# Kernel tuning notes

Hardware: AMD Instinct MI355X
Metric: run time of the kernel (lower is better)

## Reference

```python
import jax, jax.numpy as jnp
import numpy as np

DIM = 1024
HEADS = 16
MLP = 4096
EPS = 1e-5

def _layer_norm(x, g, b):
    mu = jnp.mean(x, axis=-1, keepdims=True)
    var = jnp.mean(jnp.square(x - mu), axis=-1, keepdims=True)
    return (x - mu) * jax.lax.rsqrt(var + EPS) * g + b

def setup_inputs() -> dict:
    key = jax.random.key(0)
    ks = jax.random.split(key, 8)
    s = 0.02
    return {
        "x": jax.random.normal(ks[0], (2, 2048, DIM), dtype=jnp.float32),
        "ln1_g": jnp.ones((DIM,), jnp.float32),
        "ln1_b": jnp.zeros((DIM,), jnp.float32),
        "qkv_w": jax.random.normal(ks[1], (DIM, 3 * DIM), jnp.float32) * s,
        "qkv_b": jnp.zeros((3 * DIM,), jnp.float32),
        "proj_w": jax.random.normal(ks[2], (DIM, DIM), jnp.float32) * s,
        "proj_b": jnp.zeros((DIM,), jnp.float32),
        "ln2_g": jnp.ones((DIM,), jnp.float32),
        "ln2_b": jnp.zeros((DIM,), jnp.float32),
        "fc1_w": jax.random.normal(ks[3], (DIM, MLP), jnp.float32) * s,
        "fc1_b": jnp.zeros((MLP,), jnp.float32),
        "fc2_w": jax.random.normal(ks[4], (MLP, DIM), jnp.float32) * s,
        "fc2_b": jnp.zeros((DIM,), jnp.float32),
    }

def reference(x, ln1_g, ln1_b, qkv_w, qkv_b, proj_w, proj_b,
              ln2_g, ln2_b, fc1_w, fc1_b, fc2_w, fc2_b):
    B, N, C = x.shape
    H = HEADS
    D = C // H
    # --- attention (pre-norm); NOTE: source applies no 1/sqrt(D) scaling ---
    h = _layer_norm(x, ln1_g, ln1_b)
    qkv = (h @ qkv_w + qkv_b).reshape(B, N, 3, H, D)
    q, k, v = (qkv[:, :, 0], qkv[:, :, 1], qkv[:, :, 2])  # [B,N,H,D]
    qk = jnp.einsum('bnhd,bmhd->bhnm', q, k)
    attn = jax.nn.softmax(qk, axis=-1)
    y = jnp.einsum('bhnm,bmhd->bnhd', attn, v).reshape(B, N, C)
    y = y @ proj_w + proj_b
    x = x + y
    # --- MLP (pre-norm), exact GELU like torch nn.GELU ---
    h2 = _layer_norm(x, ln2_g, ln2_b)
    h2 = jax.nn.gelu(h2 @ fc1_w + fc1_b, approximate=False)
    x = x + (h2 @ fc2_w + fc2_b)
    return x
```

## Files before the change

kernel.cpp:

```cpp
#include <hip/hip_runtime.h>
#include <hip/hip_bf16.h>

#define CDIM   1024
#define NSEQ   2048
#define NHEAD  16
#define HDIM   64
#define MLPDIM 4096
#define TROWS  4096

typedef __attribute__((ext_vector_type(8)))  __bf16 bf16x8;
typedef __attribute__((ext_vector_type(4)))  float  f32x4;
typedef __attribute__((ext_vector_type(16))) float  f32x16;
typedef __attribute__((ext_vector_type(4)))  unsigned short us4;

static __device__ __forceinline__ unsigned short f2bf(float f) {
  unsigned int u = __float_as_uint(f);
  u += 0x7fffu + ((u >> 16) & 1u);
  return (unsigned short)(u >> 16);
}

#define MFMA16(a, b, c) __builtin_amdgcn_mfma_f32_16x16x32_bf16(a, b, c, 0, 0, 0)
#define MFMA32(a, b, c) __builtin_amdgcn_mfma_f32_32x32x16_bf16(a, b, c, 0, 0, 0)

static __device__ __forceinline__ void gll16(const unsigned short* g, unsigned short* l) {
  __builtin_amdgcn_global_load_lds(
      (const __attribute__((address_space(1))) unsigned int*)g,
      (__attribute__((address_space(3))) unsigned int*)l, 16, 0, 0);
}

__global__ __launch_bounds__(256)
void ln_bf16_kernel(const float* __restrict__ x,
                    const float* __restrict__ gam,
                    const float* __restrict__ bet,
                    unsigned short* __restrict__ out)
{
  int row = blockIdx.x;
  int t = threadIdx.x;
  const float4* xr = (const float4*)(x + (size_t)row * CDIM);
  float4 v = xr[t];
  float s  = v.x + v.y + v.z + v.w;
  float s2 = v.x*v.x + v.y*v.y + v.z*v.z + v.w*v.w;
  #pragma unroll
  for (int off = 32; off > 0; off >>= 1) {
    s  += __shfl_down(s, off);
    s2 += __shfl_down(s2, off);
  }
  __shared__ float rs[4], rs2[4];
  int wave = t >> 6, lane = t & 63;
  if (lane == 0) { rs[wave] = s; rs2[wave] = s2; }
  __syncthreads();
  float fs  = rs[0] + rs[1] + rs[2] + rs[3];
  float fs2 = rs2[0] + rs2[1] + rs2[2] + rs2[3];
  float mu   = fs * (1.0f / CDIM);
  float var  = fs2 * (1.0f / CDIM) - mu * mu;
  float rstd = rsqrtf(var + 1e-5f);
  float4 gg = ((const float4*)gam)[t];
  float4 bb = ((const float4*)bet)[t];
  us4 o;
  o.x = f2bf((v.x - mu) * rstd * gg.x + bb.x);
  o.y = f2bf((v.y - mu) * rstd * gg.y + bb.y);
  o.z = f2bf((v.z - mu) * rstd * gg.z + bb.z);
  o.w = f2bf((v.w - mu) * rstd * gg.w + bb.w);
  ((us4*)(out + (size_t)row * CDIM))[t] = o;
}

__global__ __launch_bounds__(256)
void wt_bf16_kernel(const float* __restrict__ W, unsigned short* __restrict__ Wt,
                    int K, int N)
{
  __shared__ float tile[32][33];
  int n0 = blockIdx.x * 32, k0 = blockIdx.y * 32;
  int t = threadIdx.x;
  int r = t >> 3, c4 = (t & 7) << 2;
  float4 v = *(const float4*)(W + (size_t)(k0 + r) * N + n0 + c4);
  tile[r][c4 + 0] = v.x; tile[r][c4 + 1] = v.y;
  tile[r][c4 + 2] = v.z; tile[r][c4 + 3] = v.w;
  __syncthreads();
  us4 o;
  o.x = f2bf(tile[c4 + 0][r]);
  o.y = f2bf(tile[c4 + 1][r]);
  o.z = f2bf(tile[c4 + 2][r]);
  o.w = f2bf(tile[c4 + 3][r]);
  *(us4*)(Wt + (size_t)(n0 + r) * K + k0 + c4) = o;
}

template<int EPI>
__global__ __launch_bounds__(256, 2)
void gemm_bt(const unsigned short* __restrict__ A, const unsigned short* __restrict__ Bt,
             const float* __restrict__ bias, int M, int N, int K,
             float* __restrict__ outf, unsigned short* __restrict__ outb,
             const float* __restrict__ resid,
             unsigned short* __restrict__ qo, unsigned short* __restrict__ ko,
             unsigned short* __restrict__ vo)
{
  __shared__ unsigned short As[128 * 32];
  __shared__ unsigned short Bs[128 * 32];
  const int tid  = threadIdx.x;
  const int lane = tid & 63;
  const int wave = tid >> 6;
  const int wr = wave >> 1, wc = wave & 1;
  const int g = lane >> 4, r16 = lane & 15;
  const int bm = blockIdx.y * 128, bn = blockIdx.x * 128;

  f32x4 acc[4][4];
  #pragma unroll
  for (int i = 0; i < 4; i++)
    #pragma unroll
    for (int j = 0; j < 4; j++) acc[i][j] = (f32x4){0.f, 0.f, 0.f, 0.f};

  for (int k0 = 0; k0 < K; k0 += 32) {
    #pragma unroll
    for (int c = 0; c < 2; c++) {
      int o   = (c * 256 + tid) << 3;
      int row = o >> 5;
      int col = o & 31;
      int ub  = (c * 256 + (tid & ~63)) << 3;
      gll16(A  + (size_t)(bm + row) * K + k0 + col, &As[ub]);
      gll16(Bt + (size_t)(bn + row) * K + k0 + col, &Bs[ub]);
    }
    __syncthreads();
    bf16x8 af[4], bfr[4];
    #pragma unroll
    for (int i = 0; i < 4; i++) {
      int row = wr * 64 + i * 16 + r16;
      af[i] = *(const bf16x8*)(&As[row * 32 + 8 * g]);
    }
    #pragma unroll
    for (int j = 0; j < 4; j++) {
      int row = wc * 64 + j * 16 + r16;
      bfr[j] = *(const bf16x8*)(&Bs[row * 32 + 8 * g]);
    }
    #pragma unroll
    for (int i = 0; i < 4; i++)
      #pragma unroll
      for (int j = 0; j < 4; j++)
        acc[i][j] = MFMA16(af[i], bfr[j], acc[i][j]);
    __syncthreads();
  }

  #pragma unroll
  for (int i = 0; i < 4; i++) {
    #pragma unroll
    for (int j = 0; j < 4; j++) {
      int col = bn + wc * 64 + j * 16 + r16;
      float bv = bias[col];
      #pragma unroll
      for (int jj = 0; jj < 4; jj++) {
        int row = bm + wr * 64 + i * 16 + 4 * g + jj;
        float val = acc[i][j][jj] + bv;
        if (EPI == 1) {
          int sel = col >> 10, cc = col & 1023;
          int hh = cc >> 6, d = cc & 63;
          int b = row >> 11, tk = row & 2047;
          size_t hb = (size_t)(b * NHEAD + hh);
          if (sel == 0)      qo[(hb * NSEQ + tk) * HDIM + d] = f2bf(val * 1.4426950408889634f);
          else if (sel == 1) ko[(hb * NSEQ + tk) * HDIM + d] = f2bf(val);
          else               vo[(hb * HDIM + d) * NSEQ + tk] = f2bf(val);
        } else if (EPI == 2) {
          size_t idx = (size_t)row * N + col;
          outf[idx] = val + resid[idx];
        } else {
          float ge = 0.5f * val * (1.0f + erff(val * 0.70710678118654752f));
          outb[(size_t)row * N + col] = f2bf(ge);
        }
      }
    }
  }
}

__global__ __launch_bounds__(256, 2)
void attn_kernel(const unsigned short* __restrict__ q, const unsigned short* __restrict__ k,
                 const unsigned short* __restrict__ vt, unsigned short* __restrict__ y)
{
  int bid = blockIdx.x;
  int xcd = bid & 7, loc = bid >> 3;
  int bh  = xcd * 4 + (loc >> 4);
  int qblk = loc & 15;
  int b = bh >> 4, h = bh & 15;
  int wave = threadIdx.x >> 6, lane = threadIdx.x & 63;
  int ql = lane & 31;
  int hi = lane >> 5;
  int q0 = qblk * 128 + wave * 32;
  const unsigned short* qb = q  + (size_t)bh * NSEQ * HDIM;
  const unsigned short* kb = k  + (size_t)bh * NSEQ * HDIM;
  const unsigned short* vb = vt + (size_t)bh * HDIM * NSEQ;

  bf16x8 aq[4];
  #pragma unroll
  for (int s = 0; s < 4; s++)
    aq[s] = *(const bf16x8*)(qb + (size_t)(q0 + ql) * HDIM + s * 16 + hi * 8);

  float m = -1e30f, ssum = 0.f;
  f32x16 o0, o1;
  #pragma unroll
  for (int r = 0; r < 16; r++) { o0[r] = 0.f; o1[r] = 0.f; }

  bf16x8 kf[2][4];
  #pragma unroll
  for (int s = 0; s < 4; s++)
    kf[0][s] = *(const bf16x8*)(kb + (size_t)ql * HDIM + s * 16 + hi * 8);

  #pragma unroll 2
  for (int it = 0; it < NSEQ / 32; it++) {
    const int kv0 = it * 32;
    const int cur = it & 1, nxt = cur ^ 1;
    bf16x8 vf[2][2];
    #pragma unroll
    for (int t = 0; t < 2; t++)
      #pragma unroll
      for (int db = 0; db < 2; db++)
        vf[t][db] = *(const bf16x8*)(vb + (size_t)(db * 32 + ql) * NSEQ + kv0 + t * 16 + hi * 8);
    f32x16 sacc;
    #pragma unroll
    for (int r = 0; r < 16; r++) sacc[r] = 0.f;
    __builtin_amdgcn_s_setprio(1);
    #pragma unroll
    for (int s = 0; s < 4; s++)
      sacc = MFMA32(kf[cur][s], aq[s], sacc);
    __builtin_amdgcn_s_setprio(0);
    {
      int kvn = (kv0 + 32) & (NSEQ - 1);
      #pragma unroll
      for (int s = 0; s < 4; s++)
        kf[nxt][s] = *(const bf16x8*)(kb + (size_t)(kvn + ql) * HDIM + s * 16 + hi * 8);
    }
    float tmax = sacc[0];
    #pragma unroll
    for (int r = 1; r < 16; r++) tmax = fmaxf(tmax, sacc[r]);
    tmax = fmaxf(tmax, __shfl_xor(tmax, 32));
    float mn = fmaxf(m, tmax);
    float scale = exp2f(m - mn);
    m = mn;
    float ps = 0.f;
    #pragma unroll
    for (int r = 0; r < 16; r++) {
      sacc[r] = exp2f(sacc[r] - mn);
      ps += sacc[r];
    }
    ssum = ssum * scale + ps;
    #pragma unroll
    for (int r = 0; r < 16; r++) { o0[r] *= scale; o1[r] *= scale; }
    __builtin_amdgcn_s_setprio(1);
    #pragma unroll
    for (int t = 0; t < 2; t++) {
      unsigned pk01, pk23, pk45, pk67;
      asm("v_cvt_pk_bf16_f32 %0, %1, %2" : "=v"(pk01) : "v"(sacc[8*t+0]), "v"(sacc[8*t+1]));
      asm("v_cvt_pk_bf16_f32 %0, %1, %2" : "=v"(pk23) : "v"(sacc[8*t+2]), "v"(sacc[8*t+3]));
      asm("v_cvt_pk_bf16_f32 %0, %1, %2" : "=v"(pk45) : "v"(sacc[8*t+4]), "v"(sacc[8*t+5]));
      asm("v_cvt_pk_bf16_f32 %0, %1, %2" : "=v"(pk67) : "v"(sacc[8*t+6]), "v"(sacc[8*t+7]));
      asm("v_permlane32_swap_b32 %0, %1" : "+v"(pk01), "+v"(pk45));
      asm("v_permlane32_swap_b32 %0, %1" : "+v"(pk23), "+v"(pk67));
      union { unsigned u[4]; bf16x8 v; } pf;
      pf.u[0] = pk01; pf.u[1] = pk23; pf.u[2] = pk45; pf.u[3] = pk67;
      o0 = MFMA32(vf[t][0], pf.v, o0);
      o1 = MFMA32(vf[t][1], pf.v, o1);
    }
    __builtin_amdgcn_s_setprio(0);
  }
  float stot = ssum + __shfl_xor(ssum, 32);
  float inv = 1.0f / stot;
  unsigned short* yr = y + ((size_t)(b * NSEQ + q0 + ql)) * CDIM + h * HDIM;
  #pragma unroll
  for (int db = 0; db < 2; db++) {
    const f32x16& oo = db ? o1 : o0;
    #pragma unroll
    for (int rq = 0; rq < 4; rq++) {
      us4 w;
      w.x = f2bf(oo[4*rq+0] * inv);
      w.y = f2bf(oo[4*rq+1] * inv);
      w.z = f2bf(oo[4*rq+2] * inv);
      w.w = f2bf(oo[4*rq+3] * inv);
      *(us4*)(yr + db * 32 + rq * 8 + hi * 4) = w;
    }
  }
}

extern "C" void kernel_launch(void* const* d_in, const int* in_sizes, int n_in,
                              void* d_out, int out_size, void* d_ws, size_t ws_size,
                              hipStream_t stream)
{
  const float* x      = (const float*)d_in[0];
  const float* ln1_g  = (const float*)d_in[1];
  const float* ln1_b  = (const float*)d_in[2];
  const float* qkv_w  = (const float*)d_in[3];
  const float* qkv_b  = (const float*)d_in[4];
  const float* proj_w = (const float*)d_in[5];
  const float* proj_b = (const float*)d_in[6];
  const float* ln2_g  = (const float*)d_in[7];
  const float* ln2_b  = (const float*)d_in[8];
  const float* fc1_w  = (const float*)d_in[9];
  const float* fc1_b  = (const float*)d_in[10];
  const float* fc2_w  = (const float*)d_in[11];
  const float* fc2_b  = (const float*)d_in[12];
  float* out = (float*)d_out;

  char* p = (char*)d_ws;
  size_t off = 0;
  auto alloc = [&](size_t bytes) -> void* {
    void* r = p + off; off += (bytes + 255) & ~(size_t)255; return r;
  };
  unsigned short* wt_qkv  = (unsigned short*)alloc((size_t)3072 * 1024 * 2);
  unsigned short* wt_proj = (unsigned short*)alloc((size_t)1024 * 1024 * 2);
  unsigned short* wt_fc1  = (unsigned short*)alloc((size_t)4096 * 1024 * 2);
  unsigned short* wt_fc2  = (unsigned short*)alloc((size_t)1024 * 4096 * 2);
  unsigned short* h1  = (unsigned short*)alloc((size_t)TROWS * CDIM * 2);
  unsigned short* qb  = (unsigned short*)alloc((size_t)TROWS * CDIM * 2);
  unsigned short* kb  = (unsigned short*)alloc((size_t)TROWS * CDIM * 2);
  unsigned short* vtb = (unsigned short*)alloc((size_t)TROWS * CDIM * 2);
  unsigned short* yb  = (unsigned short*)alloc((size_t)TROWS * CDIM * 2);
  float*          x1  = (float*)alloc((size_t)TROWS * CDIM * 4);
  unsigned short* h2  = (unsigned short*)alloc((size_t)TROWS * CDIM * 2);
  unsigned short* g1  = (unsigned short*)alloc((size_t)TROWS * MLPDIM * 2);

  dim3 blk(256);
  wt_bf16_kernel<<<dim3(3072 / 32, 1024 / 32), blk, 0, stream>>>(qkv_w, wt_qkv, 1024, 3072);
  wt_bf16_kernel<<<dim3(1024 / 32, 1024 / 32), blk, 0, stream>>>(proj_w, wt_proj, 1024, 1024);
  wt_bf16_kernel<<<dim3(4096 / 32, 1024 / 32), blk, 0, stream>>>(fc1_w, wt_fc1, 1024, 4096);
  wt_bf16_kernel<<<dim3(1024 / 32, 4096 / 32), blk, 0, stream>>>(fc2_w, wt_fc2, 4096, 1024);
  ln_bf16_kernel<<<TROWS, blk, 0, stream>>>(x, ln1_g, ln1_b, h1);
  gemm_bt<1><<<dim3(3072 / 128, TROWS / 128), blk, 0, stream>>>(
      h1, wt_qkv, qkv_b, TROWS, 3072, 1024,
      nullptr, nullptr, nullptr, qb, kb, vtb);
  attn_kernel<<<dim3(512), blk, 0, stream>>>(qb, kb, vtb, yb);
  gemm_bt<2><<<dim3(1024 / 128, TROWS / 128), blk, 0, stream>>>(
      yb, wt_proj, proj_b, TROWS, 1024, 1024,
      x1, nullptr, x, nullptr, nullptr, nullptr);
  ln_bf16_kernel<<<TROWS, blk, 0, stream>>>(x1, ln2_g, ln2_b, h2);
  gemm_bt<3><<<dim3(MLPDIM / 128, TROWS / 128), blk, 0, stream>>>(
      h2, wt_fc1, fc1_b, TROWS, MLPDIM, 1024,
      nullptr, g1, nullptr, nullptr, nullptr, nullptr);
  gemm_bt<2><<<dim3(1024 / 128, TROWS / 128), blk, 0, stream>>>(
      g1, wt_fc2, fc2_b, TROWS, 1024, MLPDIM,
      out, nullptr, x1, nullptr, nullptr, nullptr);
}
```

Measured before the change: 342.5 us.

## Split attention KV range across wave pairs and merge partial softmax in LDS

The attention kernel now assigns each 32-row query tile to two waves that each process half of the key/value sequence (flash-decoding style split-K). Each block covers 64 queries instead of 128, so the grid doubles to 1024 blocks. The partial outputs, maxima and sums from the second wave pass through shared memory and are merged with rescaling by the first wave. The aim is more parallelism and occupancy (launch bounds raised to 4 blocks per CU) at the cost of an LDS round trip, a block-wide sync, and more register pressure under the tighter launch bound.

```diff
diff --git a/kernel.cpp b/kernel.cpp
--- a/kernel.cpp
+++ b/kernel.cpp
@@ -168,23 +168,28 @@
   }
 }
 
-__global__ __launch_bounds__(256, 2)
+__global__ __launch_bounds__(256, 4)
 void attn_kernel(const unsigned short* __restrict__ q, const unsigned short* __restrict__ k,
                  const unsigned short* __restrict__ vt, unsigned short* __restrict__ y)
 {
   int bid = blockIdx.x;
   int xcd = bid & 7, loc = bid >> 3;
-  int bh  = xcd * 4 + (loc >> 4);
-  int qblk = loc & 15;
+  int bh  = xcd * 4 + (loc >> 5);
+  int qb64 = loc & 31;
   int b = bh >> 4, h = bh & 15;
   int wave = threadIdx.x >> 6, lane = threadIdx.x & 63;
+  int qt = wave >> 1, kvh = wave & 1;
   int ql = lane & 31;
   int hi = lane >> 5;
-  int q0 = qblk * 128 + wave * 32;
+  int q0 = qb64 * 64 + qt * 32;
+  const int kvbase = kvh * (NSEQ / 2);
   const unsigned short* qb = q  + (size_t)bh * NSEQ * HDIM;
   const unsigned short* kb = k  + (size_t)bh * NSEQ * HDIM;
   const unsigned short* vb = vt + (size_t)bh * HDIM * NSEQ;
 
+  __shared__ float OM[2][64 * 33];
+  __shared__ float MSm[2][32], MSs[2][32];
+
   bf16x8 aq[4];
   #pragma unroll
   for (int s = 0; s < 4; s++)
@@ -198,11 +203,11 @@
   bf16x8 kf[2][4];
   #pragma unroll
   for (int s = 0; s < 4; s++)
-    kf[0][s] = *(const bf16x8*)(kb + (size_t)ql * HDIM + s * 16 + hi * 8);
+    kf[0][s] = *(const bf16x8*)(kb + (size_t)(kvbase + ql) * HDIM + s * 16 + hi * 8);
 
   #pragma unroll 2
-  for (int it = 0; it < NSEQ / 32; it++) {
-    const int kv0 = it * 32;
+  for (int it = 0; it < NSEQ / 64; it++) {
+    const int kv0 = kvbase + it * 32;
     const int cur = it & 1, nxt = cur ^ 1;
     bf16x8 vf[2][2];
     #pragma unroll
@@ -219,7 +224,7 @@
       sacc = MFMA32(kf[cur][s], aq[s], sacc);
     __builtin_amdgcn_s_setprio(0);
     {
-      int kvn = (kv0 + 32) & (NSEQ - 1);
+      int kvn = kvbase + ((it * 32 + 32) & (NSEQ / 2 - 1));
       #pragma unroll
       for (int s = 0; s < 4; s++)
         kf[nxt][s] = *(const bf16x8*)(kb + (size_t)(kvn + ql) * HDIM + s * 16 + hi * 8);
@@ -258,19 +263,34 @@
     __builtin_amdgcn_s_setprio(0);
   }
   float stot = ssum + __shfl_xor(ssum, 32);
-  float inv = 1.0f / stot;
-  unsigned short* yr = y + ((size_t)(b * NSEQ + q0 + ql)) * CDIM + h * HDIM;
-  #pragma unroll
-  for (int db = 0; db < 2; db++) {
-    const f32x16& oo = db ? o1 : o0;
-    #pragma unroll
-    for (int rq = 0; rq < 4; rq++) {
-      us4 w;
-      w.x = f2bf(oo[4*rq+0] * inv);
-      w.y = f2bf(oo[4*rq+1] * inv);
-      w.z = f2bf(oo[4*rq+2] * inv);
-      w.w = f2bf(oo[4*rq+3] * inv);
-      *(us4*)(yr + db * 32 + rq * 8 + hi * 4) = w;
+
+  if (kvh == 1) {
+    int base = lane * 33;
+    #pragma unroll
+    for (int r = 0; r < 16; r++) { OM[qt][base + r] = o0[r]; OM[qt][base + 16 + r] = o1[r]; }
+    if (hi == 0) { MSm[qt][ql] = m; MSs[qt][ql] = stot; }
+  }
+  __syncthreads();
+  if (kvh == 0) {
+    float m1 = MSm[qt][ql], s1 = MSs[qt][ql];
+    float mt = fmaxf(m, m1);
+    float a0 = exp2f(m - mt), a1 = exp2f(m1 - mt);
+    float inv = 1.0f / (stot * a0 + s1 * a1);
+    int base = lane * 33;
+    unsigned short* yr = y + ((size_t)(b * NSEQ + q0 + ql)) * CDIM + h * HDIM;
+    #pragma unroll
+    for (int db = 0; db < 2; db++) {
+      const f32x16& oo = db ? o1 : o0;
+      #pragma unroll
+      for (int rq = 0; rq < 4; rq++) {
+        us4 w;
+        #pragma unroll
+        for (int e = 0; e < 4; e++) {
+          float ov = oo[4*rq+e] * a0 + OM[qt][base + db*16 + 4*rq+e] * a1;
+          ((unsigned short*)&w)[e] = f2bf(ov * inv);
+        }
+        *(us4*)(yr + db * 32 + rq * 8 + hi * 4) = w;
+      }
     }
   }
 }
@@ -321,7 +341,7 @@
   gemm_bt<1><<<dim3(3072 / 128, TROWS / 128), blk, 0, stream>>>(
       h1, wt_qkv, qkv_b, TROWS, 3072, 1024,
       nullptr, nullptr, nullptr, qb, kb, vtb);
-  attn_kernel<<<dim3(512), blk, 0, stream>>>(qb, kb, vtb, yb);
+  attn_kernel<<<dim3(1024), blk, 0, stream>>>(qb, kb, vtb, yb);
   gemm_bt<2><<<dim3(1024 / 128, TROWS / 128), blk, 0, stream>>>(
       yb, wt_proj, proj_b, TROWS, 1024, 1024,
       x1, nullptr, x, nullptr, nullptr, nullptr);
```

Result: no change. 344.6 us (+0.6%).

## Stage K and V tiles through swizzled LDS with double buffering in attention

Applied to the files above, without the earlier changes.

The attention kernel now loads each 32-key K tile and V^T tile once per block into shared memory, using direct global-to-LDS loads (gll16) with an XOR swizzle. Double buffering prefetches the next tile while the current one is consumed. Previously each of the four waves loaded K and V from global memory into registers on its own, so the same data was fetched four times per block. The change adds a __syncthreads per iteration and LDS reads, and it drops the register prefetch of K and the unroll-by-two.

```diff
diff --git a/kernel.cpp b/kernel.cpp
--- a/kernel.cpp
+++ b/kernel.cpp
@@ -175,16 +175,35 @@
   int bid = blockIdx.x;
   int xcd = bid & 7, loc = bid >> 3;
   int bh  = xcd * 4 + (loc >> 4);
-  int qblk = loc & 15;
+  int qchunk = loc & 15;
   int b = bh >> 4, h = bh & 15;
   int wave = threadIdx.x >> 6, lane = threadIdx.x & 63;
   int ql = lane & 31;
   int hi = lane >> 5;
-  int q0 = qblk * 128 + wave * 32;
+  int q0 = qchunk * 128 + wave * 32;
   const unsigned short* qb = q  + (size_t)bh * NSEQ * HDIM;
   const unsigned short* kb = k  + (size_t)bh * NSEQ * HDIM;
   const unsigned short* vb = vt + (size_t)bh * HDIM * NSEQ;
 
+  __shared__ unsigned short KL[2][2048];
+  __shared__ unsigned short VL[2][2048];
+
+  auto stage = [&](int d, int it) {
+    int kv0 = it * 32;
+    {
+      int c = wave * 64 + lane;
+      int row = c >> 3, col = c & 7;
+      int sc  = (row << 3) | (col ^ (row & 7));
+      gll16(kb + (size_t)kv0 * HDIM + sc * 8, &KL[d][wave * 512]);
+    }
+    {
+      int c = wave * 64 + lane;
+      int row = c >> 2, col = c & 3;
+      int scol = col ^ ((row >> 1) & 3);
+      gll16(vb + (size_t)row * NSEQ + kv0 + scol * 8, &VL[d][wave * 512]);
+    }
+  };
+
   bf16x8 aq[4];
   #pragma unroll
   for (int s = 0; s < 4; s++)
@@ -195,35 +214,24 @@
   #pragma unroll
   for (int r = 0; r < 16; r++) { o0[r] = 0.f; o1[r] = 0.f; }
 
-  bf16x8 kf[2][4];
-  #pragma unroll
-  for (int s = 0; s < 4; s++)
-    kf[0][s] = *(const bf16x8*)(kb + (size_t)ql * HDIM + s * 16 + hi * 8);
-
-  #pragma unroll 2
+  stage(0, 0);
   for (int it = 0; it < NSEQ / 32; it++) {
-    const int kv0 = it * 32;
-    const int cur = it & 1, nxt = cur ^ 1;
-    bf16x8 vf[2][2];
-    #pragma unroll
-    for (int t = 0; t < 2; t++)
-      #pragma unroll
-      for (int db = 0; db < 2; db++)
-        vf[t][db] = *(const bf16x8*)(vb + (size_t)(db * 32 + ql) * NSEQ + kv0 + t * 16 + hi * 8);
+    const int cur = it & 1;
+    __syncthreads();
+    if (it + 1 < NSEQ / 32) stage(cur ^ 1, it + 1);
+    bf16x8 kf[4];
+    #pragma unroll
+    for (int s = 0; s < 4; s++)
+      kf[s] = *(const bf16x8*)((const char*)KL[cur] +
+               ql * 128 + ((((s << 1) | hi) ^ (ql & 7)) << 4));
     f32x16 sacc;
     #pragma unroll
     for (int r = 0; r < 16; r++) sacc[r] = 0.f;
     __builtin_amdgcn_s_setprio(1);
     #pragma unroll
     for (int s = 0; s < 4; s++)
-      sacc = MFMA32(kf[cur][s], aq[s], sacc);
+      sacc = MFMA32(kf[s], aq[s], sacc);
     __builtin_amdgcn_s_setprio(0);
-    {
-      int kvn = (kv0 + 32) & (NSEQ - 1);
-      #pragma unroll
-      for (int s = 0; s < 4; s++)
-        kf[nxt][s] = *(const bf16x8*)(kb + (size_t)(kvn + ql) * HDIM + s * 16 + hi * 8);
-    }
     float tmax = sacc[0];
     #pragma unroll
     for (int r = 1; r < 16; r++) tmax = fmaxf(tmax, sacc[r]);
@@ -240,6 +248,13 @@
     ssum = ssum * scale + ps;
     #pragma unroll
     for (int r = 0; r < 16; r++) { o0[r] *= scale; o1[r] *= scale; }
+    bf16x8 vf[2][2];
+    #pragma unroll
+    for (int t = 0; t < 2; t++)
+      #pragma unroll
+      for (int db = 0; db < 2; db++)
+        vf[t][db] = *(const bf16x8*)((const char*)VL[cur] +
+                     (db * 32 + ql) * 64 + ((((t << 1) | hi) ^ ((ql >> 1) & 3)) << 4));
     __builtin_amdgcn_s_setprio(1);
     #pragma unroll
     for (int t = 0; t < 2; t++) {
```

After: 300.7 us. -12.2%, faster.
